# Performance work log

Hardware: AMD Instinct MI355X
Metric: run time of the kernel (lower is better)

Reference implementation:

```python
import jax, jax.numpy as jnp
import numpy as np

B, E, N = 4, 100000, 10000          # batch copies, edges, nodes
NR, H, D, OUT, L = 6, 256, 256, 128, 3  # num_radial, hidden, out_emb, out, num_layers


def setup_inputs() -> dict:
    key = jax.random.key(0)
    ks = jax.random.split(key, 7)
    x = jax.random.normal(ks[0], (B, E, H), dtype=jnp.float32)
    rbf = jax.random.normal(ks[1], (E, NR), dtype=jnp.float32)
    i = jax.random.randint(ks[2], (E,), 0, N, dtype=jnp.int32)
    # Learned params (stored transposed vs torch Linear: [in, out])
    W_rbf = jax.random.normal(ks[3], (NR, H), dtype=jnp.float32) / np.float32(np.sqrt(NR))
    W_up = jax.random.normal(ks[4], (H, D), dtype=jnp.float32) / np.float32(np.sqrt(H))
    Ws = jax.random.normal(ks[5], (L, D, D), dtype=jnp.float32) / np.float32(np.sqrt(D))
    bs = jnp.zeros((L, D), dtype=jnp.float32)
    W_out = jax.random.normal(ks[6], (D, OUT), dtype=jnp.float32) / np.float32(np.sqrt(D))
    return {"x": x, "rbf": rbf, "i": i, "W_rbf": W_rbf, "W_up": W_up,
            "Ws": Ws, "bs": bs, "W_out": W_out, "num_nodes": N}


def reference(x, rbf, i, W_rbf, W_up, Ws, bs, W_out, num_nodes):
    # x: [B,E,H], rbf: [E,NR], i: [E]
    g = (rbf @ W_rbf)[None, :, :] * x            # lin_rbf(rbf) * x -> [B,E,H]
    # scatter-sum over edges into nodes (dim=1)
    agg = jax.vmap(lambda xb: jax.ops.segment_sum(xb, i, num_segments=num_nodes))(g)  # [B,N,H]
    h = agg @ W_up                               # lin_up (no bias) -> [B,N,D]
    for l in range(Ws.shape[0]):                 # small fixed layer stack
        h = jax.nn.silu(h @ Ws[l] + bs[l])
    return h @ W_out                             # lin (no bias) -> [B,N,OUT]
```

## Files before the change

kernel.cpp:

```cpp
#include <hip/hip_runtime.h>
#include <hip/hip_bf16.h>

#define B_  4
#define E_  100000
#define N_  10000
#define NR_ 6
#define H_  256
#define D_  256
#define OUT_ 128

typedef __attribute__((ext_vector_type(4))) float f32x4;
typedef __attribute__((ext_vector_type(8))) short bf16x8;

__device__ __forceinline__ ushort f2bf(float f) {
  unsigned u = __builtin_bit_cast(unsigned, f);
  u += 0x7fffu + ((u >> 16) & 1u);
  return (ushort)(u >> 16);
}

__global__ __launch_bounds__(256) void hist_convert_kernel(
    const int* __restrict__ idx, int* __restrict__ counts,
    const float* __restrict__ W_up, const float* __restrict__ Ws,
    const float* __restrict__ W_out, ushort* __restrict__ Wp) {
  if (blockIdx.x < 391) {
    const int e = blockIdx.x * 256 + threadIdx.x;
    if (e < E_) atomicAdd(&counts[idx[e]], 1);
    return;
  }
  const int g = (blockIdx.x - 391) * 256 + threadIdx.x;
  int l, goff, Ncols;
  if (g < 32768) { l = g >> 13; goff = g & 8191; Ncols = 256; }
  else           { l = 4;       goff = g - 32768; Ncols = 128; }
  const float* src = (l == 0) ? W_up : (l < 4 ? Ws + (l - 1) * 65536 : W_out);
  const int lane = goff & 63;
  const int ks   = (goff >> 6) & 7;
  const int nb   = goff >> 9;
  const int col  = nb * 16 + (lane & 15);
  const int k0   = ks * 32 + (lane >> 4) * 8;
  ushort tmp[8];
#pragma unroll
  for (int j = 0; j < 8; ++j)
    tmp[j] = f2bf(src[(size_t)(k0 + j) * Ncols + col]);
  *reinterpret_cast<uint4*>(&Wp[(size_t)g * 8]) =
      *reinterpret_cast<const uint4*>(tmp);
}

__global__ __launch_bounds__(1024) void scan_kernel(
    const int* __restrict__ counts, int* __restrict__ starts,
    int* __restrict__ cursor) {
  __shared__ int sums[1024];
  const int t = threadIdx.x;
  const int base = t * 10;
  int loc[10];
  int s = 0;
#pragma unroll
  for (int j = 0; j < 10; ++j) {
    int v = (base + j < N_) ? counts[base + j] : 0;
    loc[j] = v;
    s += v;
  }
  sums[t] = s;
  __syncthreads();
  for (int off = 1; off < 1024; off <<= 1) {
    int v = (t >= off) ? sums[t - off] : 0;
    __syncthreads();
    sums[t] += v;
    __syncthreads();
  }
  int run = sums[t] - s;
#pragma unroll
  for (int j = 0; j < 10; ++j) {
    if (base + j < N_) {
      starts[base + j] = run;
      cursor[base + j] = run;
      run += loc[j];
    }
  }
}

__global__ __launch_bounds__(256) void fill_kernel(const int* __restrict__ idx,
                                                   int* __restrict__ cursor,
                                                   int* __restrict__ buckets) {
  int e = blockIdx.x * 256 + threadIdx.x;
  if (e < E_) {
    int pos = atomicAdd(&cursor[idx[e]], 1);
    buckets[pos] = e;
  }
}

__global__ __launch_bounds__(256) void gather_kernel(
    const float* __restrict__ x, const float* __restrict__ rbf,
    const float* __restrict__ W_rbf, const int* __restrict__ starts,
    const int* __restrict__ counts, const int* __restrict__ buckets,
    ushort* __restrict__ agg) {
  const int tid = threadIdx.x;
  const int node = blockIdx.x * 4 + (tid >> 6);
  const int lane = tid & 63;
  const int h0 = lane * 4;

  f32x4 wrv[NR_];
#pragma unroll
  for (int r = 0; r < NR_; ++r)
    wrv[r] = *reinterpret_cast<const f32x4*>(&W_rbf[r * H_ + h0]);

  f32x4 acc[B_] = {};
  const int s = starts[node];
  const int d = counts[node];

#pragma unroll 2
  for (int j = 0; j < d; ++j) {
    const int e = buckets[s + j];
    f32x4 rp = {0.f, 0.f, 0.f, 0.f};
#pragma unroll
    for (int r = 0; r < NR_; ++r) rp += rbf[e * NR_ + r] * wrv[r];
#pragma unroll
    for (int b = 0; b < B_; ++b) {
      const f32x4 xv = *reinterpret_cast<const f32x4*>(
          &x[((size_t)b * E_ + e) * H_ + h0]);
      acc[b] += xv * rp;
    }
  }

#pragma unroll
  for (int b = 0; b < B_; ++b) {
    ushort4 o;
    o.x = f2bf(acc[b].x); o.y = f2bf(acc[b].y);
    o.z = f2bf(acc[b].z); o.w = f2bf(acc[b].w);
    *reinterpret_cast<ushort4*>(&agg[((size_t)b * N_ + node) * H_ + h0]) = o;
  }
}

__global__ __launch_bounds__(512) void chain_kernel(
    const ushort* __restrict__ agg, const ushort* __restrict__ Wp,
    const float* __restrict__ bs, float* __restrict__ out) {
  __shared__ ushort act[64 * 256];
  char* actb = reinterpret_cast<char*>(act);
  const int row0 = blockIdx.x * 64;
  const int tid = threadIdx.x;
  const int wave = tid >> 6;
  const int lane = tid & 63;
  const int lr = lane & 15;
  const int lq = lane >> 4;
  const int wr = wave >> 2;
  const int wc = wave & 3;

#pragma unroll
  for (int t = 0; t < 4; ++t) {
    const int idx = tid + t * 512;
    const int row = idx >> 5;
    const int s = idx & 31;
    const uint4 v = *reinterpret_cast<const uint4*>(
        &agg[(size_t)(row0 + row) * 256 + s * 8]);
    const int byte = (row * 512 + s * 16) ^ ((row & 7) << 4);
    *reinterpret_cast<uint4*>(actb + byte) = v;
  }
  __syncthreads();

  for (int l = 0; l < 4; ++l) {
    const ushort* W = Wp + l * 65536;
    f32x4 acc[2][4] = {};
#pragma unroll
    for (int ks = 0; ks < 8; ++ks) {
      bf16x8 af[2], bfr[4];
#pragma unroll
      for (int m = 0; m < 2; ++m) {
        const int row = wr * 32 + m * 16 + lr;
        const int byte = (row * 512 + ks * 64 + lq * 16) ^ ((row & 7) << 4);
        af[m] = *reinterpret_cast<const bf16x8*>(actb + byte);
      }
#pragma unroll
      for (int n = 0; n < 4; ++n) {
        const int nb = wc * 4 + n;
        bfr[n] = *reinterpret_cast<const bf16x8*>(
            &W[(size_t)(((nb * 8 + ks) * 64) + lane) * 8]);
      }
#pragma unroll
      for (int m = 0; m < 2; ++m)
#pragma unroll
        for (int n = 0; n < 4; ++n)
          acc[m][n] = __builtin_amdgcn_mfma_f32_16x16x32_bf16(af[m], bfr[n],
                                                              acc[m][n], 0, 0, 0);
    }
    __syncthreads();

    const bool ba = (l > 0);
#pragma unroll
    for (int n = 0; n < 4; ++n) {
      const int col = wc * 64 + n * 16 + lr;
      const float bv = ba ? bs[(l - 1) * 256 + col] : 0.f;
#pragma unroll
      for (int m = 0; m < 2; ++m) {
#pragma unroll
        for (int r = 0; r < 4; ++r) {
          float v = acc[m][n][r];
          if (ba) {
            v += bv;
            v = v / (1.0f + __expf(-v));
          }
          const int row = wr * 32 + m * 16 + lq * 4 + r;
          const int byte = (row * 512 + col * 2) ^ ((row & 7) << 4);
          *reinterpret_cast<ushort*>(actb + byte) = f2bf(v);
        }
      }
    }
    __syncthreads();
  }

  {
    const ushort* W = Wp + 4 * 65536;
    f32x4 acc[2][2] = {};
#pragma unroll
    for (int ks = 0; ks < 8; ++ks) {
      bf16x8 af[2], bfr[2];
#pragma unroll
      for (int m = 0; m < 2; ++m) {
        const int row = wr * 32 + m * 16 + lr;
        const int byte = (row * 512 + ks * 64 + lq * 16) ^ ((row & 7) << 4);
        af[m] = *reinterpret_cast<const bf16x8*>(actb + byte);
      }
#pragma unroll
      for (int n = 0; n < 2; ++n) {
        const int nb = wc * 2 + n;
        bfr[n] = *reinterpret_cast<const bf16x8*>(
            &W[(size_t)(((nb * 8 + ks) * 64) + lane) * 8]);
      }
#pragma unroll
      for (int m = 0; m < 2; ++m)
#pragma unroll
        for (int n = 0; n < 2; ++n)
          acc[m][n] = __builtin_amdgcn_mfma_f32_16x16x32_bf16(af[m], bfr[n],
                                                              acc[m][n], 0, 0, 0);
    }
#pragma unroll
    for (int m = 0; m < 2; ++m)
#pragma unroll
      for (int n = 0; n < 2; ++n)
#pragma unroll
        for (int r = 0; r < 4; ++r) {
          const int row = row0 + wr * 32 + m * 16 + lq * 4 + r;
          const int col = wc * 32 + n * 16 + lr;
          out[(size_t)row * OUT_ + col] = acc[m][n][r];
        }
  }
}

extern "C" void kernel_launch(void* const* d_in, const int* in_sizes, int n_in,
                              void* d_out, int out_size, void* d_ws,
                              size_t ws_size, hipStream_t stream) {
  const float* x     = (const float*)d_in[0];
  const float* rbf   = (const float*)d_in[1];
  const int*   idx   = (const int*)d_in[2];
  const float* W_rbf = (const float*)d_in[3];
  const float* W_up  = (const float*)d_in[4];
  const float* Ws    = (const float*)d_in[5];
  const float* bs    = (const float*)d_in[6];
  const float* W_out = (const float*)d_in[7];
  float* out = (float*)d_out;

  char* ws = (char*)d_ws;
  const size_t agg_bytes = (size_t)B_ * N_ * H_ * sizeof(ushort);
  ushort* agg = (ushort*)(ws);
  ushort* Wp  = (ushort*)(ws + agg_bytes);
  char* ibase = ws + agg_bytes + 294912 * sizeof(ushort);
  int* counts  = (int*)(ibase);
  int* starts  = (int*)(ibase + 40000);
  int* cursor  = (int*)(ibase + 80000);
  int* buckets = (int*)(ibase + 120000);

  hipMemsetAsync(counts, 0, N_ * sizeof(int), stream);
  hist_convert_kernel<<<391 + 144, 256, 0, stream>>>(idx, counts, W_up, Ws,
                                                     W_out, Wp);
  scan_kernel<<<1, 1024, 0, stream>>>(counts, starts, cursor);
  fill_kernel<<<(E_ + 255) / 256, 256, 0, stream>>>(idx, cursor, buckets);

  gather_kernel<<<N_ / 4, 256, 0, stream>>>(x, rbf, W_rbf, starts, counts,
                                            buckets, agg);

  chain_kernel<<<625, 512, 0, stream>>>(agg, Wp, bs, out);
}
```

Before: 199.6 us.

## Fuse edge gather into MLP chain kernel and use wave-shuffle scan

Merges the gather/scatter-sum kernel with the MLP chain kernel. Each 512-thread block computes its 64 aggregated rows directly into swizzled LDS, which removes the bf16 agg round trip through global memory and one launch. The scan kernel also replaces its LDS Hillis-Steele loop with wave shuffles plus a small cross-wave step. In exchange, each row now handles a single batch copy, so the per-edge rbf projection is recomputed once per batch. Gather work per block is also uneven because node degrees differ, and that may stall the MFMA phase.

```diff
diff --git a/kernel.cpp b/kernel.cpp
--- a/kernel.cpp
+++ b/kernel.cpp
@@ -48,8 +48,11 @@
 __global__ __launch_bounds__(1024) void scan_kernel(
     const int* __restrict__ counts, int* __restrict__ starts,
     int* __restrict__ cursor) {
-  __shared__ int sums[1024];
+  __shared__ int wsum[16];
+  __shared__ int wpre[16];
   const int t = threadIdx.x;
+  const int lane = t & 63;
+  const int w = t >> 6;
   const int base = t * 10;
   int loc[10];
   int s = 0;
@@ -59,15 +62,26 @@
     loc[j] = v;
     s += v;
   }
-  sums[t] = s;
+  int v = s;
+#pragma unroll
+  for (int off = 1; off < 64; off <<= 1) {
+    int u = __shfl_up(v, off, 64);
+    if (lane >= off) v += u;
+  }
+  if (lane == 63) wsum[w] = v;
   __syncthreads();
-  for (int off = 1; off < 1024; off <<= 1) {
-    int v = (t >= off) ? sums[t - off] : 0;
-    __syncthreads();
-    sums[t] += v;
-    __syncthreads();
-  }
-  int run = sums[t] - s;
+  if (w == 0) {
+    int wv = (lane < 16) ? wsum[lane] : 0;
+    int vv = wv;
+#pragma unroll
+    for (int off = 1; off < 16; off <<= 1) {
+      int u = __shfl_up(vv, off, 64);
+      if (lane >= off) vv += u;
+    }
+    if (lane < 16) wpre[lane] = vv - wv;
+  }
+  __syncthreads();
+  int run = wpre[w] + (v - s);
 #pragma unroll
   for (int j = 0; j < 10; ++j) {
     if (base + j < N_) {
@@ -88,73 +102,55 @@
   }
 }
 
-__global__ __launch_bounds__(256) void gather_kernel(
+__global__ __launch_bounds__(512) void fused_kernel(
     const float* __restrict__ x, const float* __restrict__ rbf,
     const float* __restrict__ W_rbf, const int* __restrict__ starts,
     const int* __restrict__ counts, const int* __restrict__ buckets,
-    ushort* __restrict__ agg) {
-  const int tid = threadIdx.x;
-  const int node = blockIdx.x * 4 + (tid >> 6);
-  const int lane = tid & 63;
-  const int h0 = lane * 4;
-
-  f32x4 wrv[NR_];
-#pragma unroll
-  for (int r = 0; r < NR_; ++r)
-    wrv[r] = *reinterpret_cast<const f32x4*>(&W_rbf[r * H_ + h0]);
-
-  f32x4 acc[B_] = {};
-  const int s = starts[node];
-  const int d = counts[node];
-
-#pragma unroll 2
-  for (int j = 0; j < d; ++j) {
-    const int e = buckets[s + j];
-    f32x4 rp = {0.f, 0.f, 0.f, 0.f};
-#pragma unroll
-    for (int r = 0; r < NR_; ++r) rp += rbf[e * NR_ + r] * wrv[r];
-#pragma unroll
-    for (int b = 0; b < B_; ++b) {
-      const f32x4 xv = *reinterpret_cast<const f32x4*>(
-          &x[((size_t)b * E_ + e) * H_ + h0]);
-      acc[b] += xv * rp;
-    }
-  }
-
-#pragma unroll
-  for (int b = 0; b < B_; ++b) {
-    ushort4 o;
-    o.x = f2bf(acc[b].x); o.y = f2bf(acc[b].y);
-    o.z = f2bf(acc[b].z); o.w = f2bf(acc[b].w);
-    *reinterpret_cast<ushort4*>(&agg[((size_t)b * N_ + node) * H_ + h0]) = o;
-  }
-}
-
-__global__ __launch_bounds__(512) void chain_kernel(
-    const ushort* __restrict__ agg, const ushort* __restrict__ Wp,
-    const float* __restrict__ bs, float* __restrict__ out) {
+    const ushort* __restrict__ Wp, const float* __restrict__ bs,
+    float* __restrict__ out) {
   __shared__ ushort act[64 * 256];
   char* actb = reinterpret_cast<char*>(act);
   const int row0 = blockIdx.x * 64;
   const int tid = threadIdx.x;
   const int wave = tid >> 6;
   const int lane = tid & 63;
+  const int h0 = lane * 4;
+
+  f32x4 wrv[NR_];
+#pragma unroll
+  for (int r = 0; r < NR_; ++r)
+    wrv[r] = *reinterpret_cast<const f32x4*>(&W_rbf[r * H_ + h0]);
+
+#pragma unroll
+  for (int i = 0; i < 8; ++i) {
+    const int row = row0 + wave * 8 + i;
+    const int b = row / N_;
+    const int node = row - b * N_;
+    const int s = starts[node];
+    const int d = counts[node];
+    f32x4 acc = {0.f, 0.f, 0.f, 0.f};
+#pragma unroll 4
+    for (int j = 0; j < d; ++j) {
+      const int e = __builtin_amdgcn_readfirstlane(buckets[s + j]);
+      f32x4 rp = {0.f, 0.f, 0.f, 0.f};
+#pragma unroll
+      for (int r = 0; r < NR_; ++r) rp += rbf[e * NR_ + r] * wrv[r];
+      const f32x4 xv = *reinterpret_cast<const f32x4*>(
+          &x[((size_t)b * E_ + e) * H_ + h0]);
+      acc += xv * rp;
+    }
+    const int lr_ = wave * 8 + i;
+    ushort4 o;
+    o.x = f2bf(acc.x); o.y = f2bf(acc.y); o.z = f2bf(acc.z); o.w = f2bf(acc.w);
+    const int byte = (lr_ * 512 + h0 * 2) ^ ((lr_ & 7) << 4);
+    *reinterpret_cast<ushort4*>(actb + byte) = o;
+  }
+  __syncthreads();
+
   const int lr = lane & 15;
   const int lq = lane >> 4;
   const int wr = wave >> 2;
   const int wc = wave & 3;
-
-#pragma unroll
-  for (int t = 0; t < 4; ++t) {
-    const int idx = tid + t * 512;
-    const int row = idx >> 5;
-    const int s = idx & 31;
-    const uint4 v = *reinterpret_cast<const uint4*>(
-        &agg[(size_t)(row0 + row) * 256 + s * 8]);
-    const int byte = (row * 512 + s * 16) ^ ((row & 7) << 4);
-    *reinterpret_cast<uint4*>(actb + byte) = v;
-  }
-  __syncthreads();
 
   for (int l = 0; l < 4; ++l) {
     const ushort* W = Wp + l * 65536;
@@ -258,10 +254,8 @@
   float* out = (float*)d_out;
 
   char* ws = (char*)d_ws;
-  const size_t agg_bytes = (size_t)B_ * N_ * H_ * sizeof(ushort);
-  ushort* agg = (ushort*)(ws);
-  ushort* Wp  = (ushort*)(ws + agg_bytes);
-  char* ibase = ws + agg_bytes + 294912 * sizeof(ushort);
+  ushort* Wp = (ushort*)ws;
+  char* ibase = ws + 294912 * sizeof(ushort);
   int* counts  = (int*)(ibase);
   int* starts  = (int*)(ibase + 40000);
   int* cursor  = (int*)(ibase + 80000);
@@ -273,8 +267,6 @@
   scan_kernel<<<1, 1024, 0, stream>>>(counts, starts, cursor);
   fill_kernel<<<(E_ + 255) / 256, 256, 0, stream>>>(idx, cursor, buckets);
 
-  gather_kernel<<<N_ / 4, 256, 0, stream>>>(x, rbf, W_rbf, starts, counts,
-                                            buckets, agg);
-
-  chain_kernel<<<625, 512, 0, stream>>>(agg, Wp, bs, out);
-}
+  fused_kernel<<<625, 512, 0, stream>>>(x, rbf, W_rbf, starts, counts, buckets,
+                                        Wp, bs, out);
+}
```

Result: slower. 303.2 us (+51.9%).
